# Kernel optimization log

Measured on AMD Instinct MI355X. Metric: run time of the kernel, lower is better.

Reference implementation:

```python
import jax, jax.numpy as jnp
import numpy as np

B, S, DIM = 2, 2048, 2048
H = 16
Q_RANK, KV_RANK = 512, 512
D_NOPE, D_ROPE, D_V = 128, 64, 128
D_QK = D_NOPE + D_ROPE  # 192
EPS = 1e-6
SCALE = D_QK ** -0.5


def setup_inputs() -> dict:
    key = jax.random.key(0)
    ks = jax.random.split(key, 8)
    x = jax.random.normal(ks[0], (B, S, DIM), dtype=jnp.float32)
    # real RoPE table: theta_i = 10000^{-2i/d}, angles = pos * theta
    inv_freq = 1.0 / (10000.0 ** (np.arange(0, D_ROPE, 2, dtype=np.float32) / D_ROPE))
    ang = np.arange(S, dtype=np.float32)[:, None] * inv_freq[None, :]  # (S, D_ROPE//2)
    freqs_cis = jnp.asarray(np.stack([np.cos(ang), np.sin(ang)], axis=-1))  # (S, 32, 2)
    std = 0.02
    wq_a = jax.random.normal(ks[1], (Q_RANK, DIM), dtype=jnp.float32) * std
    wq_b = jax.random.normal(ks[2], (H * D_QK, Q_RANK), dtype=jnp.float32) * std
    wkv_a = jax.random.normal(ks[3], (KV_RANK + D_ROPE, DIM), dtype=jnp.float32) * std
    wkv_b = jax.random.normal(ks[4], (H * (D_NOPE + D_V), KV_RANK), dtype=jnp.float32) * std
    wo = jax.random.normal(ks[5], (DIM, H * D_V), dtype=jnp.float32) * std
    q_norm_w = jnp.ones((Q_RANK,), dtype=jnp.float32)
    kv_norm_w = jnp.ones((KV_RANK,), dtype=jnp.float32)
    return {"x": x, "freqs_cis": freqs_cis, "wq_a": wq_a, "wq_b": wq_b,
            "q_norm_w": q_norm_w, "wkv_a": wkv_a, "kv_norm_w": kv_norm_w,
            "wkv_b": wkv_b, "wo": wo}


def _rmsnorm(x, w):
    var = jnp.mean(jnp.square(x), axis=-1, keepdims=True)
    return x * jax.lax.rsqrt(var + EPS) * w


def _rope(x, freqs_cis):
    # x: (B, S, h, d); freqs_cis: (S, d//2, 2) as (cos, sin). Pairs are interleaved (x0,x1),(x2,x3),...
    xr, xi = x[..., 0::2], x[..., 1::2]
    cos = freqs_cis[None, :, None, :, 0]
    sin = freqs_cis[None, :, None, :, 1]
    yr = xr * cos - xi * sin
    yi = xr * sin + xi * cos
    return jnp.stack([yr, yi], axis=-1).reshape(x.shape)


def reference(x, freqs_cis, wq_a, wq_b, q_norm_w, wkv_a, kv_norm_w, wkv_b, wo):
    b, s, _ = x.shape
    # low-rank Q projection: wq_a -> RMSNorm -> wq_b
    q = _rmsnorm(x @ wq_a.T, q_norm_w) @ wq_b.T
    q = q.reshape(b, s, H, D_QK)
    q_nope, q_pe = q[..., :D_NOPE], q[..., D_NOPE:]
    q = jnp.concatenate([q_nope, _rope(q_pe, freqs_cis)], axis=-1)  # (b,s,H,192)
    # KV path
    kv = x @ wkv_a.T  # (b,s,KV_RANK+D_ROPE)
    kv_lat, k_pe = kv[..., :KV_RANK], kv[..., KV_RANK:]
    k_pe = _rope(k_pe[:, :, None, :], freqs_cis)  # (b,s,1,64)
    kv = (_rmsnorm(kv_lat, kv_norm_w) @ wkv_b.T).reshape(b, s, H, D_NOPE + D_V)
    k_nope, v = kv[..., :D_NOPE], kv[..., D_NOPE:]
    k = jnp.concatenate([k_nope, jnp.broadcast_to(k_pe, (b, s, H, D_ROPE))], axis=-1)
    # causal scaled-dot-product attention
    scores = jnp.einsum('bshd,bthd->bhst', q, k) * SCALE
    mask = jnp.tril(jnp.ones((s, s), dtype=bool))
    scores = jnp.where(mask[None, None], scores, jnp.finfo(scores.dtype).min)
    probs = jax.nn.softmax(scores, axis=-1)
    out = jnp.einsum('bhst,bthd->bshd', probs, v).reshape(b, s, H * D_V)
    return out @ wo.T
```

## Files before the change

kernel.cpp:

```cpp
#include <hip/hip_runtime.h>
#include <cstdint>
#include <cstddef>


typedef unsigned short u16;
typedef unsigned int u32;
typedef unsigned long long u64;
typedef __attribute__((ext_vector_type(8))) short bf16x8;
typedef __attribute__((ext_vector_type(4))) float floatx4;

#define MFMA16x16x32 __builtin_amdgcn_mfma_f32_16x16x32_bf16

#define QSCALE 0.10411755f
#define THR_L2 11.541560f

__device__ __forceinline__ u16 f2bf(float f) {
  u32 u = __float_as_uint(f);
  u32 r = (u + 0x7fffu + ((u >> 16) & 1u)) >> 16;
  return (u16)r;
}

__device__ __forceinline__ void gload16(const void* g, void* l) {
  __builtin_amdgcn_global_load_lds(
      (const __attribute__((address_space(1))) void*)g,
      (__attribute__((address_space(3))) void*)l, 16, 0, 0);
}

__global__ __launch_bounds__(256) void cvt_all(
    const float* __restrict__ s0, const float* __restrict__ s1,
    const float* __restrict__ s2, const float* __restrict__ s3,
    const float* __restrict__ s4, const float* __restrict__ s5,
    u16* __restrict__ d0, u16* __restrict__ d1, u16* __restrict__ d2,
    u16* __restrict__ d3, u16* __restrict__ d4, u16* __restrict__ d5) {
  constexpr int ST1 = 2097152;
  constexpr int ST2 = ST1 + 262144;
  constexpr int ST3 = ST2 + 294912;
  constexpr int ST4 = ST3 + 393216;
  constexpr int ST5 = ST4 + 524288;
  constexpr int TOT = ST5 + 1048576;
  int i = blockIdx.x * 256 + threadIdx.x;
  int stride = gridDim.x * 256;
  for (; i < TOT; i += stride) {
    const float* sp;
    u16* dp;
    int j;
    if (i < ST1)      { sp = s0; dp = d0; j = i; }
    else if (i < ST2) { sp = s1; dp = d1; j = i - ST1; }
    else if (i < ST3) { sp = s2; dp = d2; j = i - ST2; }
    else if (i < ST4) { sp = s3; dp = d3; j = i - ST3; }
    else if (i < ST5) { sp = s4; dp = d4; j = i - ST4; }
    else              { sp = s5; dp = d5; j = i - ST5; }
    float4 v = ((const float4*)sp)[j];
    ushort4 o;
    o.x = f2bf(v.x); o.y = f2bf(v.y); o.z = f2bf(v.z); o.w = f2bf(v.w);
    ((ushort4*)dp)[j] = o;
  }
}

template <int BN>
__global__ __launch_bounds__(256) void gemm_bt(const u16* __restrict__ A,
                                               const u16* __restrict__ B,
                                               float* __restrict__ C,
                                               int M, int N, int K) {
  constexpr int FN = BN / 32;
  constexpr int BL = BN / 64;
  __shared__ alignas(16) u16 As[2][128 * 32];
  __shared__ alignas(16) u16 Bs[2][BN * 32];
  const int m0 = blockIdx.y * 128, n0 = blockIdx.x * BN;
  const int t = threadIdx.x;
  const int wv = t >> 6, lane = t & 63, g = lane >> 4, qq = lane & 15;
  const int wr = wv >> 1, wc = wv & 1;
  const int fsw = (qq >> 1) & 3;
  size_t aoff[2], boff[BL];
#pragma unroll
  for (int i = 0; i < 2; ++i) {
    int seg = t + i * 256;
    int row = seg >> 2, sl = seg & 3;
    aoff[i] = (size_t)(m0 + row) * K + (sl ^ ((row >> 1) & 3)) * 8;
  }
#pragma unroll
  for (int i = 0; i < BL; ++i) {
    int seg = t + i * 256;
    int row = seg >> 2, sl = seg & 3;
    boff[i] = (size_t)(n0 + row) * K + (sl ^ ((row >> 1) & 3)) * 8;
  }
  const floatx4 fz = {0.f, 0.f, 0.f, 0.f};
  floatx4 acc[4][FN];
#pragma unroll
  for (int m = 0; m < 4; ++m)
#pragma unroll
    for (int n = 0; n < FN; ++n) acc[m][n] = fz;

#define GSTAGE(buf, k0)                                                      \
  {                                                                          \
    _Pragma("unroll") for (int i = 0; i < 2; ++i)                            \
        gload16(&A[aoff[i] + (k0)], &As[buf][(size_t)(wv * 64 + i * 256) * 8]); \
    _Pragma("unroll") for (int i = 0; i < BL; ++i)                           \
        gload16(&B[boff[i] + (k0)], &Bs[buf][(size_t)(wv * 64 + i * 256) * 8]); \
  }

  const int nk = K >> 5;
  GSTAGE(0, 0);
  for (int kt = 0; kt < nk; ++kt) {
    asm volatile("" ::: "memory");
    if (kt + 1 < nk) {
      GSTAGE((kt + 1) & 1, (kt + 1) * 32);
      if constexpr (BN == 128)
        asm volatile("s_waitcnt vmcnt(4)" ::: "memory");
      else
        asm volatile("s_waitcnt vmcnt(3)" ::: "memory");
    } else {
      asm volatile("s_waitcnt vmcnt(0)" ::: "memory");
    }
    __builtin_amdgcn_s_barrier();
    asm volatile("" ::: "memory");
    const u16* Ab = &As[kt & 1][0];
    const u16* Bb = &Bs[kt & 1][0];
    bf16x8 af[4], bfr[FN];
#pragma unroll
    for (int m = 0; m < 4; ++m)
      af[m] = *(const bf16x8*)&Ab[(wr * 64 + m * 16 + qq) * 32 + ((g ^ fsw) * 8)];
#pragma unroll
    for (int n = 0; n < FN; ++n)
      bfr[n] = *(const bf16x8*)&Bb[(wc * (BN / 2) + n * 16 + qq) * 32 + ((g ^ fsw) * 8)];
    __builtin_amdgcn_s_setprio(1);
#pragma unroll
    for (int m = 0; m < 4; ++m)
#pragma unroll
      for (int n = 0; n < FN; ++n)
        acc[m][n] = MFMA16x16x32(af[m], bfr[n], acc[m][n], 0, 0, 0);
    __builtin_amdgcn_s_setprio(0);
    asm volatile("" ::: "memory");
    __builtin_amdgcn_s_barrier();
  }
#undef GSTAGE
#pragma unroll
  for (int m = 0; m < 4; ++m)
#pragma unroll
    for (int n = 0; n < FN; ++n)
#pragma unroll
      for (int r = 0; r < 4; ++r) {
        int row = m0 + wr * 64 + m * 16 + 4 * g + r;
        int col = n0 + wc * (BN / 2) + n * 16 + qq;
        C[(size_t)row * N + col] = acc[m][n][r];
      }
}

__global__ __launch_bounds__(256) void rmsnorm_bf16(const float* __restrict__ in,
                                                    int stride,
                                                    const float* __restrict__ w,
                                                    u16* __restrict__ out) {
  const int row = blockIdx.x, t = threadIdx.x;
  __shared__ float wsum[4];
  float2 v = *(const float2*)&in[(size_t)row * stride + 2 * t];
  float ss = v.x * v.x + v.y * v.y;
#pragma unroll
  for (int off = 1; off < 64; off <<= 1) ss += __shfl_xor(ss, off);
  if ((t & 63) == 0) wsum[t >> 6] = ss;
  __syncthreads();
  float tot = wsum[0] + wsum[1] + wsum[2] + wsum[3];
  float r = rsqrtf(tot * (1.f / 512.f) + 1e-6f);
  out[(size_t)row * 512 + 2 * t] = f2bf(v.x * r * w[2 * t]);
  out[(size_t)row * 512 + 2 * t + 1] = f2bf(v.y * r * w[2 * t + 1]);
}

__global__ __launch_bounds__(256) void rope_kpe(const float* __restrict__ ap,
                                                const float* __restrict__ fc,
                                                u16* __restrict__ kpe) {
  int idx = blockIdx.x * 256 + threadIdx.x;
  int row = idx >> 5, j = idx & 31;
  int s = row & 2047;
  float xr = ap[(size_t)row * 1088 + 1024 + 2 * j];
  float xi = ap[(size_t)row * 1088 + 1024 + 2 * j + 1];
  float c = fc[(s * 32 + j) * 2], sn = fc[(s * 32 + j) * 2 + 1];
  u32 lo = f2bf(xr * c - xi * sn), hi = f2bf(xr * sn + xi * c);
  *(u32*)&kpe[(size_t)row * 64 + 2 * j] = lo | (hi << 16);
}

__global__ __launch_bounds__(256) void rope_pack_q(const float* __restrict__ qf,
                                                   const float* __restrict__ fc,
                                                   u16* __restrict__ qbf) {
  int idx = blockIdx.x * 256 + threadIdx.x;
  int j = idx % 96;
  int rh = idx / 96;
  int h = rh & 15, row = rh >> 4;
  int b = row >> 11, s = row & 2047;
  const float* src = qf + (size_t)row * 3072 + h * 192;
  u16* dst = qbf + ((size_t)(b * 16 + h) * 2048 + s) * 192;
  if (j < 64) {
    u32 lo = f2bf(src[2 * j] * QSCALE), hi = f2bf(src[2 * j + 1] * QSCALE);
    *(u32*)&dst[2 * j] = lo | (hi << 16);
  } else {
    int jp = j - 64;
    float xr = src[128 + 2 * jp], xi = src[128 + 2 * jp + 1];
    float c = fc[(s * 32 + jp) * 2], sn = fc[(s * 32 + jp) * 2 + 1];
    u32 lo = f2bf((xr * c - xi * sn) * QSCALE);
    u32 hi = f2bf((xr * sn + xi * c) * QSCALE);
    *(u32*)&dst[128 + 2 * jp] = lo | (hi << 16);
  }
}

__global__ __launch_bounds__(256) void pack_k(const float* __restrict__ kvb,
                                              const u16* __restrict__ kpe,
                                              u16* __restrict__ kbf) {
  int idx = blockIdx.x * 256 + threadIdx.x;
  int j = idx % 96;
  int rh = idx / 96;
  int h = rh & 15, row = rh >> 4;
  int b = row >> 11, s = row & 2047;
  u16* dst = kbf + ((size_t)(b * 16 + h) * 2048 + s) * 192;
  if (j < 64) {
    const float* src = kvb + (size_t)row * 4096 + h * 256;
    u32 lo = f2bf(src[2 * j]), hi = f2bf(src[2 * j + 1]);
    *(u32*)&dst[2 * j] = lo | (hi << 16);
  } else {
    int jp = j - 64;
    *(u32*)&dst[128 + 2 * jp] = *(const u32*)&kpe[(size_t)row * 64 + 2 * jp];
  }
}

__global__ __launch_bounds__(256) void transpose_v(const float* __restrict__ kvb,
                                                   u16* __restrict__ vt) {
  __shared__ u16 T[32][34];
  const int bh = blockIdx.z, b = bh >> 4, h = bh & 15;
  const int s0 = blockIdx.x * 32, d0 = blockIdx.y * 32;
  const int tx = threadIdx.x & 31, ty = threadIdx.x >> 5;
#pragma unroll
  for (int i = 0; i < 4; ++i) {
    int sl = ty + i * 8;
    float v = kvb[(size_t)(b * 2048 + s0 + sl) * 4096 + h * 256 + 128 + d0 + tx];
    T[sl][tx] = f2bf(v);
  }
  __syncthreads();
#pragma unroll
  for (int i = 0; i < 4; ++i) {
    int dl = ty + i * 8;
    vt[((size_t)bh * 128 + d0 + dl) * 2048 + s0 + tx] = T[tx][dl];
  }
}

__global__ __launch_bounds__(256, 4) void flash_attn(const u16* __restrict__ Q,
                                                     const u16* __restrict__ Kc,
                                                     const u16* __restrict__ VT,
                                                     u16* __restrict__ O) {
  __shared__ alignas(16) u16 Ks[2][32 * 192];
  __shared__ alignas(16) u16 Vs[2][128 * 32];
  const int bid = blockIdx.x;
  const int qt = 31 - (bid >> 5);
  const int bh = bid & 31;
  const int t = threadIdx.x, wv = t >> 6, lane = t & 63;
  const int g = lane >> 4, qq = lane & 15;
  const int qrow0 = qt * 64 + wv * 16;
  const int my_last = qrow0 + 15;
  const int q_glob = qrow0 + qq;
  const int nkt = 2 * qt + 2;

  int koffg[3], voffg[2];
#pragma unroll
  for (int i = 0; i < 3; ++i) {
    int seg = t + i * 256;
    int row = seg / 24, sl = seg - row * 24;
    koffg[i] = row * 192 + (sl ^ (row & 7)) * 8;
  }
#pragma unroll
  for (int i = 0; i < 2; ++i) {
    int seg = t + i * 256;
    int row = seg >> 2, sl = seg & 3;
    voffg[i] = row * 2048 + (sl ^ ((row >> 1) & 3)) * 8;
  }
  const u16* Kt0 = Kc + (size_t)bh * 2048 * 192;
  const u16* Vt0 = VT + (size_t)bh * 128 * 2048;

  bf16x8 qf[6];
  {
    const u16* qp = Q + ((size_t)bh * 2048 + qrow0 + qq) * 192;
#pragma unroll
    for (int kk = 0; kk < 6; ++kk) qf[kk] = *(const bf16x8*)&qp[kk * 32 + g * 8];
  }
  asm volatile("s_waitcnt vmcnt(0)" ::: "memory");

  const floatx4 fz = {0.f, 0.f, 0.f, 0.f};
  floatx4 oacc[8];
#pragma unroll
  for (int d = 0; d < 8; ++d) oacc[d] = fz;
  float m_run = -1e30f, l_run = 0.f;

  const int krow0 = 2 * qq;
  const int krow1 = 2 * qq + 1;
  const int xr0 = krow0 & 7, xr1 = krow1 & 7;
  const int vsw = (qq >> 1) & 3;

#define STAGE(buf, kt)                                                       \
  {                                                                          \
    const u16* Kg = Kt0 + (size_t)(kt) * (32 * 192);                         \
    const u16* Vg = Vt0 + (kt) * 32;                                         \
    _Pragma("unroll") for (int i = 0; i < 3; ++i)                            \
        gload16(Kg + koffg[i], &Ks[buf][(size_t)(wv * 64 + i * 256) * 8]);   \
    _Pragma("unroll") for (int i = 0; i < 2; ++i)                            \
        gload16(Vg + voffg[i], &Vs[buf][(size_t)(wv * 64 + i * 256) * 8]);   \
  }

  STAGE(0, 0);
  for (int kt = 0; kt < nkt; ++kt) {
    const int k0 = kt * 32;
    asm volatile("" ::: "memory");
    if (kt + 1 < nkt) {
      STAGE((kt + 1) & 1, kt + 1);
      asm volatile("s_waitcnt vmcnt(5)" ::: "memory");
    } else {
      asm volatile("s_waitcnt vmcnt(0)" ::: "memory");
    }
    __builtin_amdgcn_s_barrier();
    asm volatile("" ::: "memory");
    if (k0 <= my_last) {
      const u16* Kb = &Ks[kt & 1][0];
      const u16* Vb = &Vs[kt & 1][0];
      floatx4 s0 = fz, s1 = fz;
      __builtin_amdgcn_s_setprio(1);
#pragma unroll
      for (int kk = 0; kk < 6; ++kk) {
        int sl = kk * 4 + g;
        bf16x8 a0 = *(const bf16x8*)&Kb[krow0 * 192 + ((sl ^ xr0) * 8)];
        bf16x8 a1 = *(const bf16x8*)&Kb[krow1 * 192 + ((sl ^ xr1) * 8)];
        s0 = MFMA16x16x32(a0, qf[kk], s0, 0, 0, 0);
        s1 = MFMA16x16x32(a1, qf[kk], s1, 0, 0, 0);
      }
      __builtin_amdgcn_s_setprio(0);
      float v[8];
      if (k0 + 31 <= qrow0) {
#pragma unroll
        for (int r = 0; r < 4; ++r) {
          v[r] = s0[r];
          v[4 + r] = s1[r];
        }
      } else {
#pragma unroll
        for (int r = 0; r < 4; ++r) {
          int key0 = k0 + 8 * g + 2 * r;
          v[r] = (key0 <= q_glob) ? s0[r] : -1e30f;
          v[4 + r] = (key0 + 1 <= q_glob) ? s1[r] : -1e30f;
        }
      }
      float mx = fmaxf(fmaxf(fmaxf(v[0], v[1]), fmaxf(v[2], v[3])),
                       fmaxf(fmaxf(v[4], v[5]), fmaxf(v[6], v[7])));
      mx = fmaxf(mx, __shfl_xor(mx, 16));
      mx = fmaxf(mx, __shfl_xor(mx, 32));
      if (!__all(mx <= m_run + THR_L2)) {
        float m_new = fmaxf(m_run, mx);
        float alpha = exp2f(m_run - m_new);
        m_run = m_new;
        l_run *= alpha;
#pragma unroll
        for (int d = 0; d < 8; ++d)
#pragma unroll
          for (int r = 0; r < 4; ++r) oacc[d][r] *= alpha;
      }
      float pex[8], sum = 0.f;
#pragma unroll
      for (int i = 0; i < 8; ++i) {
        pex[i] = exp2f(v[i] - m_run);
        sum += pex[i];
      }
      sum += __shfl_xor(sum, 16);
      sum += __shfl_xor(sum, 32);
      l_run += sum;
      bf16x8 pf;
      ((u32*)&pf)[0] = (u32)f2bf(pex[0]) | ((u32)f2bf(pex[4]) << 16);
      ((u32*)&pf)[1] = (u32)f2bf(pex[1]) | ((u32)f2bf(pex[5]) << 16);
      ((u32*)&pf)[2] = (u32)f2bf(pex[2]) | ((u32)f2bf(pex[6]) << 16);
      ((u32*)&pf)[3] = (u32)f2bf(pex[3]) | ((u32)f2bf(pex[7]) << 16);
      __builtin_amdgcn_s_setprio(1);
#pragma unroll
      for (int d = 0; d < 8; ++d) {
        bf16x8 vf = *(const bf16x8*)&Vb[(d * 16 + qq) * 32 + ((g ^ vsw) * 8)];
        oacc[d] = MFMA16x16x32(vf, pf, oacc[d], 0, 0, 0);
      }
      __builtin_amdgcn_s_setprio(0);
    }
    asm volatile("" ::: "memory");
    __builtin_amdgcn_s_barrier();
  }
#undef STAGE
  float linv = 1.f / l_run;
  const int b = bh >> 4, h = bh & 15;
  size_t rowoff = ((size_t)b * 2048 + qrow0 + qq) * 2048 + h * 128 + 4 * g;
#pragma unroll
  for (int d = 0; d < 8; ++d) {
    u32 lo = (u32)f2bf(oacc[d][0] * linv) | ((u32)f2bf(oacc[d][1] * linv) << 16);
    u32 hi = (u32)f2bf(oacc[d][2] * linv) | ((u32)f2bf(oacc[d][3] * linv) << 16);
    u64 w = (u64)lo | ((u64)hi << 32);
    *(u64*)&O[rowoff + d * 16] = w;
  }
}

extern "C" void kernel_launch(void* const* d_in, const int* in_sizes, int n_in,
                              void* d_out, int out_size, void* d_ws,
                              size_t ws_size, hipStream_t stream) {
  (void)in_sizes; (void)n_in; (void)out_size;
  const float* x = (const float*)d_in[0];
  const float* fc = (const float*)d_in[1];
  const float* wqa = (const float*)d_in[2];
  const float* wqb = (const float*)d_in[3];
  const float* qnw = (const float*)d_in[4];
  const float* wkva = (const float*)d_in[5];
  const float* kvnw = (const float*)d_in[6];
  const float* wkvb = (const float*)d_in[7];
  const float* wo = (const float*)d_in[8];
  float* out = (float*)d_out;
  char* ws = (char*)d_ws;

  size_t off = 0;
  auto alloc = [&](size_t bytes) {
    size_t o = off;
    off += (bytes + 255) & ~(size_t)255;
    return o;
  };
  const size_t o_xbf = alloc(16777216);
  const size_t o_wa = alloc(4456448);
  const size_t o_wqb = alloc(3145728);
  const size_t o_wkvb = alloc(4194304);
  const size_t o_wo = alloc(8388608);
  const size_t o_qln = alloc(4194304);
  const size_t o_kvln = alloc(4194304);
  const size_t o_kpe = alloc(524288);
  const size_t o_big = alloc(67108864);
  const size_t o_qbf = alloc(25165824);
  const size_t o_kbf = alloc(25165824);
  const size_t o_vt = alloc(16777216);
  if (ws_size < off) return;

  u16* xbf = (u16*)(ws + o_xbf);
  u16* wab = (u16*)(ws + o_wa);
  u16* wqbb = (u16*)(ws + o_wqb);
  u16* wkvbb = (u16*)(ws + o_wkvb);
  u16* wob = (u16*)(ws + o_wo);
  u16* qlatn = (u16*)(ws + o_qln);
  u16* kvlatn = (u16*)(ws + o_kvln);
  u16* kpe = (u16*)(ws + o_kpe);
  float* aproj = (float*)(ws + o_big);
  float* qfull = (float*)(ws + o_big);
  float* kvb = (float*)(ws + o_big);
  u16* qbf = (u16*)(ws + o_qbf);
  u16* kbf = (u16*)(ws + o_kbf);
  u16* vt = (u16*)(ws + o_vt);
  u16* attnbf = (u16*)(ws + o_xbf);

  cvt_all<<<2048, 256, 0, stream>>>(x, wqa, wkva, wqb, wkvb, wo,
                                    xbf, wab, wab + 1048576, wqbb, wkvbb, wob);

  gemm_bt<64><<<dim3(17, 32), 256, 0, stream>>>(xbf, wab, aproj, 4096, 1088, 2048);
  rmsnorm_bf16<<<4096, 256, 0, stream>>>(aproj, 1088, qnw, qlatn);
  rmsnorm_bf16<<<4096, 256, 0, stream>>>(aproj + 512, 1088, kvnw, kvlatn);
  rope_kpe<<<512, 256, 0, stream>>>(aproj, fc, kpe);

  gemm_bt<128><<<dim3(24, 32), 256, 0, stream>>>(qlatn, wqbb, qfull, 4096, 3072, 512);
  rope_pack_q<<<24576, 256, 0, stream>>>(qfull, fc, qbf);

  gemm_bt<128><<<dim3(32, 32), 256, 0, stream>>>(kvlatn, wkvbb, kvb, 4096, 4096, 512);
  pack_k<<<24576, 256, 0, stream>>>(kvb, kpe, kbf);
  transpose_v<<<dim3(64, 4, 32), 256, 0, stream>>>(kvb, vt);

  flash_attn<<<1024, 256, 0, stream>>>(qbf, kbf, vt, attnbf);
  gemm_bt<128><<<dim3(16, 32), 256, 0, stream>>>(attnbf, wob, out, 4096, 2048, 2048);
}
```

Measured before the change: 301.8 us.

## Compute softmax row sum via MFMA, use packed bf16 converts, fix K swizzle

Replaces the per-tile exp-sum and its cross-lane shuffles with an extra MFMA that multiplies a ones vector by the bf16 probabilities, so the row-sum accumulates in a matrix accumulator. It also moves the max shuffles inside the rescale branch, which now runs only when some lane exceeds the threshold. Software bf16 rounding is swapped for the hardware v_cvt_pk_bf16_f32 instruction. The K LDS swizzle now keys on row>>1 so the two rows a lane reads share an XOR pattern, aiming to cut bank conflicts. The row sum is now taken from bf16-rounded probabilities, which changes numerics slightly.

```diff
diff --git a/kernel.cpp b/kernel.cpp
--- a/kernel.cpp
+++ b/kernel.cpp
@@ -18,6 +18,12 @@
   u32 u = __float_as_uint(f);
   u32 r = (u + 0x7fffu + ((u >> 16) & 1u)) >> 16;
   return (u16)r;
+}
+
+__device__ __forceinline__ u32 cvtpk(float lo, float hi) {
+  u32 r;
+  asm("v_cvt_pk_bf16_f32 %0, %1, %2" : "=v"(r) : "v"(lo), "v"(hi));
+  return r;
 }
 
 __device__ __forceinline__ void gload16(const void* g, void* l) {
@@ -260,7 +266,7 @@
   for (int i = 0; i < 3; ++i) {
     int seg = t + i * 256;
     int row = seg / 24, sl = seg - row * 24;
-    koffg[i] = row * 192 + (sl ^ (row & 7)) * 8;
+    koffg[i] = row * 192 + (sl ^ ((row >> 1) & 7)) * 8;
   }
 #pragma unroll
   for (int i = 0; i < 2; ++i) {
@@ -281,13 +287,18 @@
 
   const floatx4 fz = {0.f, 0.f, 0.f, 0.f};
   floatx4 oacc[8];
+  floatx4 oacc_l = fz;
 #pragma unroll
   for (int d = 0; d < 8; ++d) oacc[d] = fz;
-  float m_run = -1e30f, l_run = 0.f;
+  float m_run = -1e30f;
+
+  bf16x8 ones;
+#pragma unroll
+  for (int i = 0; i < 8; ++i) ones[i] = (short)0x3f80;
 
   const int krow0 = 2 * qq;
   const int krow1 = 2 * qq + 1;
-  const int xr0 = krow0 & 7, xr1 = krow1 & 7;
+  const int xrk = qq & 7;
   const int vsw = (qq >> 1) & 3;
 
 #define STAGE(buf, kt)                                                       \
@@ -320,8 +331,8 @@
 #pragma unroll
       for (int kk = 0; kk < 6; ++kk) {
         int sl = kk * 4 + g;
-        bf16x8 a0 = *(const bf16x8*)&Kb[krow0 * 192 + ((sl ^ xr0) * 8)];
-        bf16x8 a1 = *(const bf16x8*)&Kb[krow1 * 192 + ((sl ^ xr1) * 8)];
+        bf16x8 a0 = *(const bf16x8*)&Kb[krow0 * 192 + ((sl ^ xrk) * 8)];
+        bf16x8 a1 = *(const bf16x8*)&Kb[krow1 * 192 + ((sl ^ xrk) * 8)];
         s0 = MFMA16x16x32(a0, qf[kk], s0, 0, 0, 0);
         s1 = MFMA16x16x32(a1, qf[kk], s1, 0, 0, 0);
       }
@@ -341,53 +352,49 @@
           v[4 + r] = (key0 + 1 <= q_glob) ? s1[r] : -1e30f;
         }
       }
-      float mx = fmaxf(fmaxf(fmaxf(v[0], v[1]), fmaxf(v[2], v[3])),
-                       fmaxf(fmaxf(v[4], v[5]), fmaxf(v[6], v[7])));
-      mx = fmaxf(mx, __shfl_xor(mx, 16));
-      mx = fmaxf(mx, __shfl_xor(mx, 32));
-      if (!__all(mx <= m_run + THR_L2)) {
+      float mloc = fmaxf(fmaxf(fmaxf(v[0], v[1]), fmaxf(v[2], v[3])),
+                         fmaxf(fmaxf(v[4], v[5]), fmaxf(v[6], v[7])));
+      if (!__all(mloc <= m_run + THR_L2)) {
+        float mx = fmaxf(mloc, __shfl_xor(mloc, 16));
+        mx = fmaxf(mx, __shfl_xor(mx, 32));
         float m_new = fmaxf(m_run, mx);
         float alpha = exp2f(m_run - m_new);
         m_run = m_new;
-        l_run *= alpha;
 #pragma unroll
         for (int d = 0; d < 8; ++d)
 #pragma unroll
           for (int r = 0; r < 4; ++r) oacc[d][r] *= alpha;
+#pragma unroll
+        for (int r = 0; r < 4; ++r) oacc_l[r] *= alpha;
       }
-      float pex[8], sum = 0.f;
-#pragma unroll
-      for (int i = 0; i < 8; ++i) {
-        pex[i] = exp2f(v[i] - m_run);
-        sum += pex[i];
-      }
-      sum += __shfl_xor(sum, 16);
-      sum += __shfl_xor(sum, 32);
-      l_run += sum;
+      float pex[8];
+#pragma unroll
+      for (int i = 0; i < 8; ++i) pex[i] = exp2f(v[i] - m_run);
       bf16x8 pf;
-      ((u32*)&pf)[0] = (u32)f2bf(pex[0]) | ((u32)f2bf(pex[4]) << 16);
-      ((u32*)&pf)[1] = (u32)f2bf(pex[1]) | ((u32)f2bf(pex[5]) << 16);
-      ((u32*)&pf)[2] = (u32)f2bf(pex[2]) | ((u32)f2bf(pex[6]) << 16);
-      ((u32*)&pf)[3] = (u32)f2bf(pex[3]) | ((u32)f2bf(pex[7]) << 16);
+      ((u32*)&pf)[0] = cvtpk(pex[0], pex[4]);
+      ((u32*)&pf)[1] = cvtpk(pex[1], pex[5]);
+      ((u32*)&pf)[2] = cvtpk(pex[2], pex[6]);
+      ((u32*)&pf)[3] = cvtpk(pex[3], pex[7]);
       __builtin_amdgcn_s_setprio(1);
 #pragma unroll
       for (int d = 0; d < 8; ++d) {
         bf16x8 vf = *(const bf16x8*)&Vb[(d * 16 + qq) * 32 + ((g ^ vsw) * 8)];
         oacc[d] = MFMA16x16x32(vf, pf, oacc[d], 0, 0, 0);
       }
+      oacc_l = MFMA16x16x32(ones, pf, oacc_l, 0, 0, 0);
       __builtin_amdgcn_s_setprio(0);
     }
     asm volatile("" ::: "memory");
     __builtin_amdgcn_s_barrier();
   }
 #undef STAGE
-  float linv = 1.f / l_run;
+  float linv = 1.f / oacc_l[0];
   const int b = bh >> 4, h = bh & 15;
   size_t rowoff = ((size_t)b * 2048 + qrow0 + qq) * 2048 + h * 128 + 4 * g;
 #pragma unroll
   for (int d = 0; d < 8; ++d) {
-    u32 lo = (u32)f2bf(oacc[d][0] * linv) | ((u32)f2bf(oacc[d][1] * linv) << 16);
-    u32 hi = (u32)f2bf(oacc[d][2] * linv) | ((u32)f2bf(oacc[d][3] * linv) << 16);
+    u32 lo = cvtpk(oacc[d][0] * linv, oacc[d][1] * linv);
+    u32 hi = cvtpk(oacc[d][2] * linv, oacc[d][3] * linv);
     u64 w = (u64)lo | ((u64)hi << 32);
     *(u64*)&O[rowoff + d * 16] = w;
   }
```

Measured after the change: 289.3 us. 4.1% less time.
